# Optimization experiments

Hardware: AMD Instinct MI355X
Metric: run time of the kernel (lower is better)

## Reference

```python
import jax, jax.numpy as jnp
import numpy as np

B, C, T = 64, 8, 2048
K, DIL = 64, 1
NF = 32                      # n_frequencies (<= K//2+1 = 33)
MLP, HID = 32, 64
FFT_DIM = C * NF * 2         # 512
W = T - DIL * (K - 1)        # 1985 windows (== max_windows)


def setup_inputs() -> dict:
    key = jax.random.key(0)
    ks = jax.random.split(key, 12)
    s = 0.05
    return {
        "x": jax.random.normal(ks[0], (B, C, T), jnp.float32),
        "proj_w": jax.random.normal(ks[1], (MLP, FFT_DIM), jnp.float32) * s,
        "proj_b": jax.random.normal(ks[2], (MLP,), jnp.float32) * s,
        "w0": jax.random.normal(ks[3], (HID, MLP), jnp.float32) * s,      # Linear(32->64)
        "b0": jax.random.normal(ks[4], (HID,), jnp.float32) * s,
        "a0": jnp.ones((HID,), jnp.float32),                              # Snake a (a_init=1)
        "w1": jax.random.normal(ks[5], (MLP, HID), jnp.float32) * s,      # Linear(64->32)
        "b1": jax.random.normal(ks[6], (MLP,), jnp.float32) * s,
        "a1": jnp.ones((MLP,), jnp.float32),
        "wo": jax.random.normal(ks[7], (1, MLP), jnp.float32) * s,        # output Linear(32->1)
        "bo": jax.random.normal(ks[8], (1,), jnp.float32) * s,
        "agg": jax.random.normal(ks[9], (W,), jnp.float32) * s,           # agg_weights
    }


def _snake(x, a):
    aa = jnp.abs(a) + 1e-8
    return x + jnp.sin(aa * x) ** 2 / aa


def reference(x, proj_w, proj_b, w0, b0, a0, w1, b1, a1, wo, bo, agg):
    eff = DIL * (K - 1)
    # window t uses sorted indices t-(K-1)*DIL, ..., t  (step DIL)
    idx = eff + jnp.arange(W)[:, None] - (K - 1 - jnp.arange(K))[None, :] * DIL  # [W,K]
    win = x[:, :, idx]                                   # [B,C,W,K]
    fft = jnp.fft.rfft(win, axis=-1)[..., :NF]           # [B,C,W,NF] complex
    mag = jnp.log1p(jnp.abs(fft))
    ph = jnp.arctan2(fft.imag, fft.real) / np.pi
    feat = jnp.stack([mag, ph], axis=-1)                 # [B,C,W,NF,2]
    feat = jnp.transpose(feat, (0, 2, 1, 3, 4)).reshape(B, W, FFT_DIM)
    proj = jnp.tanh(feat @ proj_w.T + proj_b) * np.pi    # [B,W,MLP]
    h = _snake(proj @ w0.T + b0, a0)                     # [B,W,HID]
    h = _snake(h @ w1.T + b1, a1)                        # [B,W,MLP]
    out_t = (h @ wo.T + bo)[..., 0]                      # [B,W]
    wts = jax.nn.softmax(agg)                            # [W]
    return jnp.sum(out_t * wts, axis=1)                  # [B]
```

## Files before the change

kernel.cpp:

```cpp
#include <hip/hip_runtime.h>
#include <math.h>

#define B_ 64
#define C_ 8
#define T_ 2048
#define NF_ 32
#define MLP_ 32
#define HID_ 64
#define W_ 1985
#define CH_ 32
#define NCHUNK_ 63
#define PI_F 3.14159265358979323846f

typedef _Float16 f16x8 __attribute__((ext_vector_type(8)));
typedef _Float16 f16x2 __attribute__((ext_vector_type(2)));
typedef float    f32x4 __attribute__((ext_vector_type(4)));

#define WS_PARTIAL 64
#define WS_TWHI    4096
#define WS_TWLO    6144
#define WS_PWHI    8192
#define WS_PWLO    16384
#define WS_W0HI    24576
#define WS_W0LO    25600
#define WS_W1HI    26624
#define WS_W1LO    27648

__device__ __forceinline__ float fast_rcp(float x) { return __builtin_amdgcn_rcpf(x); }

__device__ __forceinline__ float fast_atan2pi(float y, float x)
{
    const float ax = fabsf(x), ay = fabsf(y);
    const float mx = fmaxf(ax, ay), mn = fminf(ax, ay);
    const float r  = mn * fast_rcp(fmaxf(mx, 1e-30f));
    const float t  = r * r;
    float a = -0.003730950f;
    a = fmaf(a, t,  0.016759940f);
    a = fmaf(a, t, -0.037059946f);
    a = fmaf(a, t,  0.061602941f);
    a = fmaf(a, t, -0.105877528f);
    a = fmaf(a, t,  0.318302656f);
    a *= r;
    a = (ay > ax) ? (0.5f - a) : a;
    a = (x < 0.0f) ? (1.0f - a) : a;
    return copysignf(a, y);
}

__device__ __forceinline__ float fast_tanh(float x)
{
    const float e = __expf(2.0f * x);
    return 1.0f - 2.0f * fast_rcp(e + 1.0f);
}

__device__ __forceinline__ float fast_snake(float h, float rcp_aa, float aa)
{
    const float s = __sinf(aa * h);
    return h + s * s * rcp_aa;
}

__device__ __forceinline__ float dot4(float4 a, float4 b, float acc)
{
    return fmaf(a.x, b.x, fmaf(a.y, b.y, fmaf(a.z, b.z, fmaf(a.w, b.w, acc))));
}

__device__ __forceinline__ unsigned packhl(float v)
{
    const _Float16 h = (_Float16)v;
    const _Float16 l = (_Float16)(v - (float)h);
    f16x2 p; p[0] = h; p[1] = l;
    return __builtin_bit_cast(unsigned, p);
}

__device__ __forceinline__ void unpack8(const unsigned* u, f16x8& ah, f16x8& al)
{
    union { unsigned w[4]; f16x8 v; } H, L;
    #pragma unroll
    for (int j = 0; j < 4; ++j) {
        H.w[j] = __builtin_amdgcn_perm(u[2*j+1], u[2*j], 0x05040100u);
        L.w[j] = __builtin_amdgcn_perm(u[2*j+1], u[2*j], 0x07060302u);
    }
    ah = H.v; al = L.v;
}

__device__ __forceinline__ void gload_lds16(const void* g, void* l)
{
    __builtin_amdgcn_global_load_lds(
        (const __attribute__((address_space(1))) void*)g,
        (__attribute__((address_space(3))) void*)l, 16, 0, 0);
}

__global__ __launch_bounds__(1024) void k_pre(
    const float* __restrict__ agg, const float* __restrict__ pw,
    const float* __restrict__ w0g, const float* __restrict__ w1g,
    float* __restrict__ ws)
{
    __shared__ float red[1024];
    const int t = threadIdx.x;

    _Float16* twHi = (_Float16*)(ws + WS_TWHI);
    _Float16* twLo = (_Float16*)(ws + WS_TWLO);
    #pragma unroll
    for (int e = 0; e < 4; ++e) {
        const int id = t * 4 + e;
        const int n = id >> 6, k = id & 63;
        const int f = n & 31;
        float s, c;
        sincosf(0.0981747704246810387f * (float)((k * f) & 63), &s, &c);
        const float v = (n < 32) ? c : -s;
        const _Float16 h = (_Float16)v;
        twHi[id] = h;
        twLo[id] = (_Float16)(v - (float)h);
    }

    _Float16* pwHi = (_Float16*)(ws + WS_PWHI);
    _Float16* pwLo = (_Float16*)(ws + WS_PWLO);
    #pragma unroll
    for (int e = 0; e < 16; ++e) {
        const int id = e * 1024 + t;
        const float v = pw[id];
        const _Float16 h = (_Float16)v;
        pwHi[id] = h;
        pwLo[id] = (_Float16)(v - (float)h);
    }

    _Float16* w0Hi = (_Float16*)(ws + WS_W0HI);
    _Float16* w0Lo = (_Float16*)(ws + WS_W0LO);
    _Float16* w1Hi = (_Float16*)(ws + WS_W1HI);
    _Float16* w1Lo = (_Float16*)(ws + WS_W1LO);
    #pragma unroll
    for (int e = 0; e < 2; ++e) {
        const int id = e * 1024 + t;
        const float v0 = w0g[id];
        const _Float16 h0 = (_Float16)v0;
        w0Hi[id] = h0;
        w0Lo[id] = (_Float16)(v0 - (float)h0);
        const float v1 = w1g[id];
        const _Float16 h1 = (_Float16)v1;
        w1Hi[id] = h1;
        w1Lo[id] = (_Float16)(v1 - (float)h1);
    }

    float m = -1e30f;
    for (int i = t; i < W_; i += 1024) m = fmaxf(m, agg[i]);
    red[t] = m;
    __syncthreads();
    for (int s = 512; s > 0; s >>= 1) {
        if (t < s) red[t] = fmaxf(red[t], red[t + s]);
        __syncthreads();
    }
    const float mx = red[0];
    __syncthreads();
    float sum = 0.f;
    for (int i = t; i < W_; i += 1024) sum += __expf(agg[i] - mx);
    red[t] = sum;
    __syncthreads();
    for (int s = 512; s > 0; s >>= 1) {
        if (t < s) red[t] += red[t + s];
        __syncthreads();
    }
    if (t == 0) { ws[0] = mx; ws[1] = red[0]; }
}

__global__ __launch_bounds__(1024, 8) void k_main(
    const float* __restrict__ x,  const float* __restrict__ pw,
    const float* __restrict__ pb, const float* __restrict__ w0g,
    const float* __restrict__ b0g,const float* __restrict__ a0g,
    const float* __restrict__ w1g,const float* __restrict__ b1g,
    const float* __restrict__ a1g,const float* __restrict__ wog,
    const float* __restrict__ bog,const float* __restrict__ agg,
    const float* __restrict__ wsp, float* __restrict__ partial)
{
    __shared__ __align__(16) _Float16 twHiL[4096];
    __shared__ __align__(16) _Float16 twLoL[4096];
    __shared__ __align__(16) _Float16 featP[16384];
    __shared__ __align__(16) _Float16 projP[2560];
    __shared__ __align__(16) _Float16 h0P[4608];
    __shared__ __align__(16) unsigned xtileP[C_][100];
    __shared__ float smalls[260];
    __shared__ float chunkAcc[CH_];

    _Float16* featHi = featP;
    _Float16* featLo = featP + 8192;
    _Float16* projHi = projP;
    _Float16* projLo = projP + 1280;
    _Float16* h0Hi   = h0P;
    _Float16* h0Lo   = h0P + 2304;
    float* pacc = (float*)featP;
    float* h1L  = (float*)featP;

    const int t     = threadIdx.x;
    const int chunk = blockIdx.x;
    const int b     = blockIdx.y;
    const int w0c   = chunk * CH_;
    const int wid   = t >> 6;
    const int lane  = t & 63;
    const int m16   = lane & 15;
    const int kl    = lane >> 4;
    const int cdft  = wid >> 1;

    {
        const int gl = (wid & 7) * 64 + lane;
        const int n  = gl >> 3, q = gl & 7;
        const int srcg = n * 8 + (q ^ (n & 7));
        const float* srcbase = wsp + ((wid < 8) ? WS_TWHI : WS_TWLO);
        _Float16* dst = ((wid < 8) ? twHiL : twLoL) + gl * 8;
        gload_lds16((const char*)srcbase + srcg * 16, dst);
    }

    if (t < C_ * 96) {
        const int c = t / 96;
        const int j = t - c * 96;
        int gi = w0c + j; if (gi > T_ - 1) gi = T_ - 1;
        xtileP[c][j] = packhl(x[((size_t)b * C_ + c) * T_ + gi]);
    }
    if (t < 257) {
        float smv;
        if      (t <  32) smv = pb[t];
        else if (t <  96) smv = b0g[t - 32];
        else if (t < 160) smv = a0g[t - 96];
        else if (t < 192) smv = b1g[t - 160];
        else if (t < 224) smv = a1g[t - 192];
        else if (t < 256) smv = wog[t - 224];
        else              smv = bog[0];
        smalls[t] = smv;
    }
    __syncthreads();

    f32x4 dacc0 = {0.f,0.f,0.f,0.f}, dacc1 = {0.f,0.f,0.f,0.f};
    f32x4 dacc2 = {0.f,0.f,0.f,0.f}, dacc3 = {0.f,0.f,0.f,0.f};
    const int wra = (wid & 1) * 16 + m16;
    {
        #pragma unroll
        for (int kstep = 0; kstep < 2; ++kstep) {
            const int kq = kstep * 4 + kl;
            unsigned ut[8];
            #pragma unroll
            for (int j = 0; j < 8; ++j) ut[j] = xtileP[cdft][wra + kq * 8 + j];
            f16x8 ah, al; unpack8(ut, ah, al);
            f32x4* dp[4] = { &dacc0, &dacc1, &dacc2, &dacc3 };
            #pragma unroll
            for (int nt = 0; nt < 4; ++nt) {
                const int nrow = nt * 16 + m16;
                const int gB = (nrow * 8 + (kq ^ (nrow & 7))) * 8;
                const f16x8 bh = *(const f16x8*)&twHiL[gB];
                const f16x8 bl = *(const f16x8*)&twLoL[gB];
                f32x4 a = *dp[nt];
                a = __builtin_amdgcn_mfma_f32_16x16x32_f16(ah, bh, a, 0, 0, 0);
                a = __builtin_amdgcn_mfma_f32_16x16x32_f16(al, bh, a, 0, 0, 0);
                a = __builtin_amdgcn_mfma_f32_16x16x32_f16(ah, bl, a, 0, 0, 0);
                *dp[nt] = a;
            }
        }
    }

    unsigned heldHi[2][4], heldLo[2][4];
    {
        const int wbase = (wid & 1) * 16 + kl * 4;
        const int ccl   = cdft & 3;
        const float reA[2][4] = {{dacc0[0],dacc0[1],dacc0[2],dacc0[3]},
                                 {dacc1[0],dacc1[1],dacc1[2],dacc1[3]}};
        const float imA[2][4] = {{dacc2[0],dacc2[1],dacc2[2],dacc2[3]},
                                 {dacc3[0],dacc3[1],dacc3[2],dacc3[3]}};
        #pragma unroll
        for (int fi = 0; fi < 2; ++fi) {
            const int f = fi * 16 + m16;
            const int g = ccl * 8 + (f >> 2);
            const int sub = 2 * (f & 3);
            #pragma unroll
            for (int r = 0; r < 4; ++r) {
                const int w  = wbase + r;
                const float re = reA[fi][r], im = imA[fi][r];
                const float mag = __logf(1.0f + __builtin_amdgcn_sqrtf(re*re + im*im));
                const float ph  = fast_atan2pi(im, re);
                const _Float16 mh = (_Float16)mag;
                const _Float16 qh = (_Float16)ph;
                f16x2 vh; vh[0] = mh; vh[1] = qh;
                f16x2 vl;
                vl[0] = (_Float16)(mag - (float)mh);
                vl[1] = (_Float16)(ph  - (float)qh);
                if (wid < 8) {
                    const int off = w * 256 + ((g ^ (w & 7)) * 8) + sub;
                    *(f16x2*)&featHi[off] = vh;
                    *(f16x2*)&featLo[off] = vl;
                } else {
                    heldHi[fi][r] = __builtin_bit_cast(unsigned, vh);
                    heldLo[fi][r] = __builtin_bit_cast(unsigned, vl);
                }
            }
        }
    }
    __syncthreads();

    const _Float16* pwHi = (const _Float16*)(wsp + WS_PWHI);
    const _Float16* pwLo = (const _Float16*)(wsp + WS_PWLO);
    {
        const int wt = (wid >> 1) & 1;
        const int ot = wid & 1;
        const int kq4 = wid >> 2;
        const int arow = wt * 16 + m16;
        const int brow = ot * 16 + m16;
        f32x4 acc = {0.f, 0.f, 0.f, 0.f};
        #pragma unroll
        for (int p = 0; p < 2; ++p) {
            #pragma unroll
            for (int kstep = 0; kstep < 2; ++kstep) {
                const int kp = kq4 * 64 + kstep * 32 + kl * 8;
                const f16x8 bh = *(const f16x8*)&pwHi[(size_t)brow * 512 + p * 256 + kp];
                const f16x8 bl = *(const f16x8*)&pwLo[(size_t)brow * 512 + p * 256 + kp];
                const int g0 = kp >> 3;
                const int offA = arow * 256 + ((g0 ^ (arow & 7)) * 8);
                const f16x8 ah = *(const f16x8*)&featHi[offA];
                const f16x8 al = *(const f16x8*)&featLo[offA];
                acc = __builtin_amdgcn_mfma_f32_16x16x32_f16(ah, bh, acc, 0, 0, 0);
                acc = __builtin_amdgcn_mfma_f32_16x16x32_f16(al, bh, acc, 0, 0, 0);
                acc = __builtin_amdgcn_mfma_f32_16x16x32_f16(ah, bl, acc, 0, 0, 0);
            }
            if (p == 0) {
                __syncthreads();
                if (wid >= 8) {
                    const int wbase = (wid & 1) * 16 + kl * 4;
                    const int ccl   = cdft & 3;
                    #pragma unroll
                    for (int fi = 0; fi < 2; ++fi) {
                        const int f = fi * 16 + m16;
                        const int g = ccl * 8 + (f >> 2);
                        const int sub = 2 * (f & 3);
                        #pragma unroll
                        for (int r = 0; r < 4; ++r) {
                            const int w  = wbase + r;
                            const int off = w * 256 + ((g ^ (w & 7)) * 8) + sub;
                            *(unsigned*)&featHi[off] = heldHi[fi][r];
                            *(unsigned*)&featLo[off] = heldLo[fi][r];
                        }
                    }
                }
                __syncthreads();
            }
        }
        __syncthreads();
        #pragma unroll
        for (int r = 0; r < 4; ++r) {
            const int w = wt * 16 + kl * 4 + r;
            const int o = ot * 16 + m16;
            pacc[kq4 * 1056 + w * 33 + o] = acc[r];
        }
    }
    __syncthreads();

    {
        const int o = t & 31;
        const int w = t >> 5;
        float s = smalls[o];
        #pragma unroll
        for (int q = 0; q < 4; ++q) s += pacc[q * 1056 + w * 33 + o];
        const float pr = fast_tanh(s) * PI_F;
        const _Float16 h = (_Float16)pr;
        projHi[w * 40 + o] = h;
        projLo[w * 40 + o] = (_Float16)(pr - (float)h);
    }
    __syncthreads();

    const _Float16* w0Hi = (const _Float16*)(wsp + WS_W0HI);
    const _Float16* w0Lo = (const _Float16*)(wsp + WS_W0LO);
    if (wid < 8) {
        const int wt = wid & 1;
        const int ot = wid >> 1;
        const int arow = wt * 16 + m16;
        const int brow = ot * 16 + m16;
        const f16x8 ah = *(const f16x8*)&projHi[arow * 40 + kl * 8];
        const f16x8 al = *(const f16x8*)&projLo[arow * 40 + kl * 8];
        const f16x8 bh = *(const f16x8*)&w0Hi[brow * 32 + kl * 8];
        const f16x8 bl = *(const f16x8*)&w0Lo[brow * 32 + kl * 8];
        f32x4 acc = {0.f, 0.f, 0.f, 0.f};
        acc = __builtin_amdgcn_mfma_f32_16x16x32_f16(ah, bh, acc, 0, 0, 0);
        acc = __builtin_amdgcn_mfma_f32_16x16x32_f16(al, bh, acc, 0, 0, 0);
        acc = __builtin_amdgcn_mfma_f32_16x16x32_f16(ah, bl, acc, 0, 0, 0);
        const int o  = ot * 16 + m16;
        const float b0v = smalls[32 + o];
        const float aa  = fabsf(smalls[96 + o]) + 1e-8f;
        const float ra  = fast_rcp(aa);
        #pragma unroll
        for (int r = 0; r < 4; ++r) {
            const int w = wt * 16 + kl * 4 + r;
            const float hv = fast_snake(acc[r] + b0v, ra, aa);
            const _Float16 h = (_Float16)hv;
            h0Hi[w * 72 + o] = h;
            h0Lo[w * 72 + o] = (_Float16)(hv - (float)h);
        }
    }
    __syncthreads();

    const _Float16* w1Hi = (const _Float16*)(wsp + WS_W1HI);
    const _Float16* w1Lo = (const _Float16*)(wsp + WS_W1LO);
    if (wid < 4) {
        const int wt = wid & 1;
        const int ot = wid >> 1;
        const int arow = wt * 16 + m16;
        const int brow = ot * 16 + m16;
        f32x4 acc = {0.f, 0.f, 0.f, 0.f};
        #pragma unroll
        for (int ks = 0; ks < 2; ++ks) {
            const f16x8 ah = *(const f16x8*)&h0Hi[arow * 72 + ks * 32 + kl * 8];
            const f16x8 al = *(const f16x8*)&h0Lo[arow * 72 + ks * 32 + kl * 8];
            const f16x8 bh = *(const f16x8*)&w1Hi[brow * 64 + ks * 32 + kl * 8];
            const f16x8 bl = *(const f16x8*)&w1Lo[brow * 64 + ks * 32 + kl * 8];
            acc = __builtin_amdgcn_mfma_f32_16x16x32_f16(ah, bh, acc, 0, 0, 0);
            acc = __builtin_amdgcn_mfma_f32_16x16x32_f16(al, bh, acc, 0, 0, 0);
            acc = __builtin_amdgcn_mfma_f32_16x16x32_f16(ah, bl, acc, 0, 0, 0);
        }
        const int o  = ot * 16 + m16;
        const float b1v = smalls[160 + o];
        const float aa  = fabsf(smalls[192 + o]) + 1e-8f;
        const float ra  = fast_rcp(aa);
        #pragma unroll
        for (int r = 0; r < 4; ++r) {
            const int w = wt * 16 + kl * 4 + r;
            h1L[w * 36 + o] = fast_snake(acc[r] + b1v, ra, aa);
        }
    }
    __syncthreads();

    if (t < CH_) {
        const int w = t;
        float acc = 0.f;
        #pragma unroll
        for (int q = 0; q < 8; ++q)
            acc = dot4(*(const float4*)&h1L[w * 36 + q * 4],
                       *(const float4*)&smalls[224 + q * 4], acc);
        const float val = acc + smalls[256];
        const int wg = w0c + w;
        const float sw = (wg < W_) ? __expf(agg[wg] - wsp[0]) / wsp[1] : 0.f;
        chunkAcc[w] = val * sw;
    }
    __syncthreads();

    if (t < 32) {
        float vs = chunkAcc[t];
        vs += __shfl_down(vs, 16);
        vs += __shfl_down(vs, 8);
        vs += __shfl_down(vs, 4);
        vs += __shfl_down(vs, 2);
        vs += __shfl_down(vs, 1);
        if (t == 0) partial[(size_t)chunk * B_ + b] = vs;
    }
}

__global__ void k_reduce(const float* __restrict__ partial, float* __restrict__ out)
{
    const int b = threadIdx.x;
    if (b < B_) {
        float s = 0.f;
        for (int c = 0; c < NCHUNK_; ++c) s += partial[(size_t)c * B_ + b];
        out[b] = s;
    }
}

extern "C" void kernel_launch(void* const* d_in, const int* in_sizes, int n_in,
                              void* d_out, int out_size, void* d_ws, size_t ws_size,
                              hipStream_t stream)
{
    const float* x   = (const float*)d_in[0];
    const float* pw  = (const float*)d_in[1];
    const float* pb  = (const float*)d_in[2];
    const float* w0  = (const float*)d_in[3];
    const float* b0  = (const float*)d_in[4];
    const float* a0  = (const float*)d_in[5];
    const float* w1  = (const float*)d_in[6];
    const float* b1  = (const float*)d_in[7];
    const float* a1  = (const float*)d_in[8];
    const float* wo  = (const float*)d_in[9];
    const float* bo  = (const float*)d_in[10];
    const float* agg = (const float*)d_in[11];
    float* ws  = (float*)d_ws;
    float* out = (float*)d_out;

    k_pre<<<1, 1024, 0, stream>>>(agg, pw, w0, w1, ws);
    dim3 grid(NCHUNK_, B_);
    k_main<<<grid, 1024, 0, stream>>>(x, pw, pb, w0, b0, a0, w1, b1, a1, wo, bo,
                                      agg, ws, ws + WS_PARTIAL);
    k_reduce<<<1, 64, 0, stream>>>(ws + WS_PARTIAL, out);
}
```

Before: 122.6 us.

## Halve block size, drop LDS twiddle staging, and alias buffers into feature tile

Changes the main kernel from 1024 to 512 threads per block. Each wave now processes two channels in sequence, alternating the DFT MFMA stage with a partial projection GEMM per channel pair. Twiddles are read straight from global/L2 instead of being copied into LDS with global_load_lds, and the proj/h0 buffers are aliased into the feature buffer to cut LDS per block. The aim is more resident blocks per CU and less LDS traffic. The cost is more barriers, serialised per-wave work, and unswizzled global twiddle reads.

```diff
diff --git a/kernel.cpp b/kernel.cpp
--- a/kernel.cpp
+++ b/kernel.cpp
@@ -82,13 +82,6 @@
     ah = H.v; al = L.v;
 }
 
-__device__ __forceinline__ void gload_lds16(const void* g, void* l)
-{
-    __builtin_amdgcn_global_load_lds(
-        (const __attribute__((address_space(1))) void*)g,
-        (__attribute__((address_space(3))) void*)l, 16, 0, 0);
-}
-
 __global__ __launch_bounds__(1024) void k_pre(
     const float* __restrict__ agg, const float* __restrict__ pw,
     const float* __restrict__ w0g, const float* __restrict__ w1g,
@@ -161,7 +154,7 @@
     if (t == 0) { ws[0] = mx; ws[1] = red[0]; }
 }
 
-__global__ __launch_bounds__(1024, 8) void k_main(
+__global__ __launch_bounds__(512, 8) void k_main(
     const float* __restrict__ x,  const float* __restrict__ pw,
     const float* __restrict__ pb, const float* __restrict__ w0g,
     const float* __restrict__ b0g,const float* __restrict__ a0g,
@@ -170,23 +163,19 @@
     const float* __restrict__ bog,const float* __restrict__ agg,
     const float* __restrict__ wsp, float* __restrict__ partial)
 {
-    __shared__ __align__(16) _Float16 twHiL[4096];
-    __shared__ __align__(16) _Float16 twLoL[4096];
     __shared__ __align__(16) _Float16 featP[16384];
-    __shared__ __align__(16) _Float16 projP[2560];
-    __shared__ __align__(16) _Float16 h0P[4608];
     __shared__ __align__(16) unsigned xtileP[C_][100];
     __shared__ float smalls[260];
     __shared__ float chunkAcc[CH_];
 
     _Float16* featHi = featP;
     _Float16* featLo = featP + 8192;
-    _Float16* projHi = projP;
-    _Float16* projLo = projP + 1280;
-    _Float16* h0Hi   = h0P;
-    _Float16* h0Lo   = h0P + 2304;
-    float* pacc = (float*)featP;
-    float* h1L  = (float*)featP;
+    float*    pacc   = (float*)featP;
+    _Float16* projHi = featP + 4224;
+    _Float16* projLo = featP + 4224 + 1280;
+    _Float16* h0Hi   = featP + 6784;
+    _Float16* h0Lo   = featP + 6784 + 2304;
+    float*    h1L    = (float*)featP;
 
     const int t     = threadIdx.x;
     const int chunk = blockIdx.x;
@@ -196,20 +185,10 @@
     const int lane  = t & 63;
     const int m16   = lane & 15;
     const int kl    = lane >> 4;
-    const int cdft  = wid >> 1;
-
-    {
-        const int gl = (wid & 7) * 64 + lane;
-        const int n  = gl >> 3, q = gl & 7;
-        const int srcg = n * 8 + (q ^ (n & 7));
-        const float* srcbase = wsp + ((wid < 8) ? WS_TWHI : WS_TWLO);
-        _Float16* dst = ((wid < 8) ? twHiL : twLoL) + gl * 8;
-        gload_lds16((const char*)srcbase + srcg * 16, dst);
-    }
-
-    if (t < C_ * 96) {
-        const int c = t / 96;
-        const int j = t - c * 96;
+
+    for (int i = t; i < C_ * 100; i += 512) {
+        const int c = i / 100;
+        const int j = i - c * 100;
         int gi = w0c + j; if (gi > T_ - 1) gi = T_ - 1;
         xtileP[c][j] = packhl(x[((size_t)b * C_ + c) * T_ + gi]);
     }
@@ -226,133 +205,125 @@
     }
     __syncthreads();
 
-    f32x4 dacc0 = {0.f,0.f,0.f,0.f}, dacc1 = {0.f,0.f,0.f,0.f};
-    f32x4 dacc2 = {0.f,0.f,0.f,0.f}, dacc3 = {0.f,0.f,0.f,0.f};
-    const int wra = (wid & 1) * 16 + m16;
-    {
+    const _Float16* twHig = (const _Float16*)(wsp + WS_TWHI);
+    const _Float16* twLog = (const _Float16*)(wsp + WS_TWLO);
+    const _Float16* pwHi  = (const _Float16*)(wsp + WS_PWHI);
+    const _Float16* pwLo  = (const _Float16*)(wsp + WS_PWLO);
+
+    const int cdl = wid >> 1;
+    const int wh  = wid & 1;
+    const int wra = wh * 16 + m16;
+    const int gwt = (wid >> 1) & 1;
+    const int got = wid & 1;
+    const int gkq = wid >> 2;
+    const int garow = gwt * 16 + m16;
+    const int gbrow = got * 16 + m16;
+    f32x4 acc = {0.f, 0.f, 0.f, 0.f};
+
+    #pragma unroll
+    for (int p = 0; p < 2; ++p) {
+        const int c = p * 4 + cdl;
+        f32x4 d0 = {0.f,0.f,0.f,0.f}, d1 = {0.f,0.f,0.f,0.f};
+        f32x4 d2 = {0.f,0.f,0.f,0.f}, d3 = {0.f,0.f,0.f,0.f};
         #pragma unroll
         for (int kstep = 0; kstep < 2; ++kstep) {
             const int kq = kstep * 4 + kl;
             unsigned ut[8];
             #pragma unroll
-            for (int j = 0; j < 8; ++j) ut[j] = xtileP[cdft][wra + kq * 8 + j];
+            for (int j = 0; j < 8; ++j) ut[j] = xtileP[c][wra + kq * 8 + j];
             f16x8 ah, al; unpack8(ut, ah, al);
-            f32x4* dp[4] = { &dacc0, &dacc1, &dacc2, &dacc3 };
+            {
+                const f16x8 bh = *(const f16x8*)&twHig[(m16     ) * 64 + kq * 8];
+                const f16x8 bl = *(const f16x8*)&twLog[(m16     ) * 64 + kq * 8];
+                d0 = __builtin_amdgcn_mfma_f32_16x16x32_f16(ah, bh, d0, 0, 0, 0);
+                d0 = __builtin_amdgcn_mfma_f32_16x16x32_f16(al, bh, d0, 0, 0, 0);
+                d0 = __builtin_amdgcn_mfma_f32_16x16x32_f16(ah, bl, d0, 0, 0, 0);
+            }
+            {
+                const f16x8 bh = *(const f16x8*)&twHig[(16 + m16) * 64 + kq * 8];
+                const f16x8 bl = *(const f16x8*)&twLog[(16 + m16) * 64 + kq * 8];
+                d1 = __builtin_amdgcn_mfma_f32_16x16x32_f16(ah, bh, d1, 0, 0, 0);
+                d1 = __builtin_amdgcn_mfma_f32_16x16x32_f16(al, bh, d1, 0, 0, 0);
+                d1 = __builtin_amdgcn_mfma_f32_16x16x32_f16(ah, bl, d1, 0, 0, 0);
+            }
+            {
+                const f16x8 bh = *(const f16x8*)&twHig[(32 + m16) * 64 + kq * 8];
+                const f16x8 bl = *(const f16x8*)&twLog[(32 + m16) * 64 + kq * 8];
+                d2 = __builtin_amdgcn_mfma_f32_16x16x32_f16(ah, bh, d2, 0, 0, 0);
+                d2 = __builtin_amdgcn_mfma_f32_16x16x32_f16(al, bh, d2, 0, 0, 0);
+                d2 = __builtin_amdgcn_mfma_f32_16x16x32_f16(ah, bl, d2, 0, 0, 0);
+            }
+            {
+                const f16x8 bh = *(const f16x8*)&twHig[(48 + m16) * 64 + kq * 8];
+                const f16x8 bl = *(const f16x8*)&twLog[(48 + m16) * 64 + kq * 8];
+                d3 = __builtin_amdgcn_mfma_f32_16x16x32_f16(ah, bh, d3, 0, 0, 0);
+                d3 = __builtin_amdgcn_mfma_f32_16x16x32_f16(al, bh, d3, 0, 0, 0);
+                d3 = __builtin_amdgcn_mfma_f32_16x16x32_f16(ah, bl, d3, 0, 0, 0);
+            }
+        }
+
+        {
+            const int cl = c & 3;
+            const int wbase = wh * 16 + kl * 4;
+            const float reA[2][4] = {{d0[0],d0[1],d0[2],d0[3]},
+                                     {d1[0],d1[1],d1[2],d1[3]}};
+            const float imA[2][4] = {{d2[0],d2[1],d2[2],d2[3]},
+                                     {d3[0],d3[1],d3[2],d3[3]}};
             #pragma unroll
-            for (int nt = 0; nt < 4; ++nt) {
-                const int nrow = nt * 16 + m16;
-                const int gB = (nrow * 8 + (kq ^ (nrow & 7))) * 8;
-                const f16x8 bh = *(const f16x8*)&twHiL[gB];
-                const f16x8 bl = *(const f16x8*)&twLoL[gB];
-                f32x4 a = *dp[nt];
-                a = __builtin_amdgcn_mfma_f32_16x16x32_f16(ah, bh, a, 0, 0, 0);
-                a = __builtin_amdgcn_mfma_f32_16x16x32_f16(al, bh, a, 0, 0, 0);
-                a = __builtin_amdgcn_mfma_f32_16x16x32_f16(ah, bl, a, 0, 0, 0);
-                *dp[nt] = a;
-            }
-        }
-    }
-
-    unsigned heldHi[2][4], heldLo[2][4];
-    {
-        const int wbase = (wid & 1) * 16 + kl * 4;
-        const int ccl   = cdft & 3;
-        const float reA[2][4] = {{dacc0[0],dacc0[1],dacc0[2],dacc0[3]},
-                                 {dacc1[0],dacc1[1],dacc1[2],dacc1[3]}};
-        const float imA[2][4] = {{dacc2[0],dacc2[1],dacc2[2],dacc2[3]},
-                                 {dacc3[0],dacc3[1],dacc3[2],dacc3[3]}};
-        #pragma unroll
-        for (int fi = 0; fi < 2; ++fi) {
-            const int f = fi * 16 + m16;
-            const int g = ccl * 8 + (f >> 2);
-            const int sub = 2 * (f & 3);
-            #pragma unroll
-            for (int r = 0; r < 4; ++r) {
-                const int w  = wbase + r;
-                const float re = reA[fi][r], im = imA[fi][r];
-                const float mag = __logf(1.0f + __builtin_amdgcn_sqrtf(re*re + im*im));
-                const float ph  = fast_atan2pi(im, re);
-                const _Float16 mh = (_Float16)mag;
-                const _Float16 qh = (_Float16)ph;
-                f16x2 vh; vh[0] = mh; vh[1] = qh;
-                f16x2 vl;
-                vl[0] = (_Float16)(mag - (float)mh);
-                vl[1] = (_Float16)(ph  - (float)qh);
-                if (wid < 8) {
+            for (int fi = 0; fi < 2; ++fi) {
+                const int f = fi * 16 + m16;
+                const int g = cl * 8 + (f >> 2);
+                const int sub = 2 * (f & 3);
+                #pragma unroll
+                for (int r = 0; r < 4; ++r) {
+                    const int w = wbase + r;
+                    const float re = reA[fi][r], im = imA[fi][r];
+                    const float mag = __logf(1.0f + __builtin_amdgcn_sqrtf(re*re + im*im));
+                    const float ph  = fast_atan2pi(im, re);
+                    const _Float16 mh = (_Float16)mag;
+                    const _Float16 qh = (_Float16)ph;
+                    f16x2 vh; vh[0] = mh; vh[1] = qh;
+                    f16x2 vl;
+                    vl[0] = (_Float16)(mag - (float)mh);
+                    vl[1] = (_Float16)(ph  - (float)qh);
                     const int off = w * 256 + ((g ^ (w & 7)) * 8) + sub;
                     *(f16x2*)&featHi[off] = vh;
                     *(f16x2*)&featLo[off] = vl;
-                } else {
-                    heldHi[fi][r] = __builtin_bit_cast(unsigned, vh);
-                    heldLo[fi][r] = __builtin_bit_cast(unsigned, vl);
                 }
             }
         }
-    }
-    __syncthreads();
-
-    const _Float16* pwHi = (const _Float16*)(wsp + WS_PWHI);
-    const _Float16* pwLo = (const _Float16*)(wsp + WS_PWLO);
-    {
-        const int wt = (wid >> 1) & 1;
-        const int ot = wid & 1;
-        const int kq4 = wid >> 2;
-        const int arow = wt * 16 + m16;
-        const int brow = ot * 16 + m16;
-        f32x4 acc = {0.f, 0.f, 0.f, 0.f};
-        #pragma unroll
-        for (int p = 0; p < 2; ++p) {
-            #pragma unroll
-            for (int kstep = 0; kstep < 2; ++kstep) {
-                const int kp = kq4 * 64 + kstep * 32 + kl * 8;
-                const f16x8 bh = *(const f16x8*)&pwHi[(size_t)brow * 512 + p * 256 + kp];
-                const f16x8 bl = *(const f16x8*)&pwLo[(size_t)brow * 512 + p * 256 + kp];
-                const int g0 = kp >> 3;
-                const int offA = arow * 256 + ((g0 ^ (arow & 7)) * 8);
-                const f16x8 ah = *(const f16x8*)&featHi[offA];
-                const f16x8 al = *(const f16x8*)&featLo[offA];
-                acc = __builtin_amdgcn_mfma_f32_16x16x32_f16(ah, bh, acc, 0, 0, 0);
-                acc = __builtin_amdgcn_mfma_f32_16x16x32_f16(al, bh, acc, 0, 0, 0);
-                acc = __builtin_amdgcn_mfma_f32_16x16x32_f16(ah, bl, acc, 0, 0, 0);
-            }
-            if (p == 0) {
-                __syncthreads();
-                if (wid >= 8) {
-                    const int wbase = (wid & 1) * 16 + kl * 4;
-                    const int ccl   = cdft & 3;
-                    #pragma unroll
-                    for (int fi = 0; fi < 2; ++fi) {
-                        const int f = fi * 16 + m16;
-                        const int g = ccl * 8 + (f >> 2);
-                        const int sub = 2 * (f & 3);
-                        #pragma unroll
-                        for (int r = 0; r < 4; ++r) {
-                            const int w  = wbase + r;
-                            const int off = w * 256 + ((g ^ (w & 7)) * 8) + sub;
-                            *(unsigned*)&featHi[off] = heldHi[fi][r];
-                            *(unsigned*)&featLo[off] = heldLo[fi][r];
-                        }
-                    }
-                }
-                __syncthreads();
-            }
-        }
         __syncthreads();
-        #pragma unroll
-        for (int r = 0; r < 4; ++r) {
-            const int w = wt * 16 + kl * 4 + r;
-            const int o = ot * 16 + m16;
-            pacc[kq4 * 1056 + w * 33 + o] = acc[r];
-        }
-    }
-    __syncthreads();
-
-    {
-        const int o = t & 31;
-        const int w = t >> 5;
-        float s = smalls[o];
-        #pragma unroll
-        for (int q = 0; q < 4; ++q) s += pacc[q * 1056 + w * 33 + o];
+
+        #pragma unroll
+        for (int kstep = 0; kstep < 4; ++kstep) {
+            const int kloc = gkq * 128 + kstep * 32 + kl * 8;
+            const f16x8 bh = *(const f16x8*)&pwHi[(size_t)gbrow * 512 + p * 256 + kloc];
+            const f16x8 bl = *(const f16x8*)&pwLo[(size_t)gbrow * 512 + p * 256 + kloc];
+            const int g0 = kloc >> 3;
+            const int offA = garow * 256 + ((g0 ^ (garow & 7)) * 8);
+            const f16x8 ah = *(const f16x8*)&featHi[offA];
+            const f16x8 al = *(const f16x8*)&featLo[offA];
+            acc = __builtin_amdgcn_mfma_f32_16x16x32_f16(ah, bh, acc, 0, 0, 0);
+            acc = __builtin_amdgcn_mfma_f32_16x16x32_f16(al, bh, acc, 0, 0, 0);
+            acc = __builtin_amdgcn_mfma_f32_16x16x32_f16(ah, bl, acc, 0, 0, 0);
+        }
+        __syncthreads();
+    }
+
+    #pragma unroll
+    for (int r = 0; r < 4; ++r) {
+        const int w = gwt * 16 + kl * 4 + r;
+        const int o = got * 16 + m16;
+        pacc[gkq * 1056 + w * 33 + o] = acc[r];
+    }
+    __syncthreads();
+
+    #pragma unroll
+    for (int q2 = 0; q2 < 2; ++q2) {
+        const int idx = t + q2 * 512;
+        const int o = idx & 31;
+        const int w = idx >> 5;
+        const float s = smalls[o] + pacc[w * 33 + o] + pacc[1056 + w * 33 + o];
         const float pr = fast_tanh(s) * PI_F;
         const _Float16 h = (_Float16)pr;
         projHi[w * 40 + o] = h;
@@ -362,7 +333,7 @@
 
     const _Float16* w0Hi = (const _Float16*)(wsp + WS_W0HI);
     const _Float16* w0Lo = (const _Float16*)(wsp + WS_W0LO);
-    if (wid < 8) {
+    {
         const int wt = wid & 1;
         const int ot = wid >> 1;
         const int arow = wt * 16 + m16;
@@ -371,10 +342,10 @@
         const f16x8 al = *(const f16x8*)&projLo[arow * 40 + kl * 8];
         const f16x8 bh = *(const f16x8*)&w0Hi[brow * 32 + kl * 8];
         const f16x8 bl = *(const f16x8*)&w0Lo[brow * 32 + kl * 8];
-        f32x4 acc = {0.f, 0.f, 0.f, 0.f};
-        acc = __builtin_amdgcn_mfma_f32_16x16x32_f16(ah, bh, acc, 0, 0, 0);
-        acc = __builtin_amdgcn_mfma_f32_16x16x32_f16(al, bh, acc, 0, 0, 0);
-        acc = __builtin_amdgcn_mfma_f32_16x16x32_f16(ah, bl, acc, 0, 0, 0);
+        f32x4 hacc = {0.f, 0.f, 0.f, 0.f};
+        hacc = __builtin_amdgcn_mfma_f32_16x16x32_f16(ah, bh, hacc, 0, 0, 0);
+        hacc = __builtin_amdgcn_mfma_f32_16x16x32_f16(al, bh, hacc, 0, 0, 0);
+        hacc = __builtin_amdgcn_mfma_f32_16x16x32_f16(ah, bl, hacc, 0, 0, 0);
         const int o  = ot * 16 + m16;
         const float b0v = smalls[32 + o];
         const float aa  = fabsf(smalls[96 + o]) + 1e-8f;
@@ -382,7 +353,7 @@
         #pragma unroll
         for (int r = 0; r < 4; ++r) {
             const int w = wt * 16 + kl * 4 + r;
-            const float hv = fast_snake(acc[r] + b0v, ra, aa);
+            const float hv = fast_snake(hacc[r] + b0v, ra, aa);
             const _Float16 h = (_Float16)hv;
             h0Hi[w * 72 + o] = h;
             h0Lo[w * 72 + o] = (_Float16)(hv - (float)h);
@@ -397,16 +368,16 @@
         const int ot = wid >> 1;
         const int arow = wt * 16 + m16;
         const int brow = ot * 16 + m16;
-        f32x4 acc = {0.f, 0.f, 0.f, 0.f};
+        f32x4 hacc = {0.f, 0.f, 0.f, 0.f};
         #pragma unroll
         for (int ks = 0; ks < 2; ++ks) {
             const f16x8 ah = *(const f16x8*)&h0Hi[arow * 72 + ks * 32 + kl * 8];
             const f16x8 al = *(const f16x8*)&h0Lo[arow * 72 + ks * 32 + kl * 8];
             const f16x8 bh = *(const f16x8*)&w1Hi[brow * 64 + ks * 32 + kl * 8];
             const f16x8 bl = *(const f16x8*)&w1Lo[brow * 64 + ks * 32 + kl * 8];
-            acc = __builtin_amdgcn_mfma_f32_16x16x32_f16(ah, bh, acc, 0, 0, 0);
-            acc = __builtin_amdgcn_mfma_f32_16x16x32_f16(al, bh, acc, 0, 0, 0);
-            acc = __builtin_amdgcn_mfma_f32_16x16x32_f16(ah, bl, acc, 0, 0, 0);
+            hacc = __builtin_amdgcn_mfma_f32_16x16x32_f16(ah, bh, hacc, 0, 0, 0);
+            hacc = __builtin_amdgcn_mfma_f32_16x16x32_f16(al, bh, hacc, 0, 0, 0);
+            hacc = __builtin_amdgcn_mfma_f32_16x16x32_f16(ah, bl, hacc, 0, 0, 0);
         }
         const int o  = ot * 16 + m16;
         const float b1v = smalls[160 + o];
@@ -415,19 +386,19 @@
         #pragma unroll
         for (int r = 0; r < 4; ++r) {
             const int w = wt * 16 + kl * 4 + r;
-            h1L[w * 36 + o] = fast_snake(acc[r] + b1v, ra, aa);
+            h1L[w * 36 + o] = fast_snake(hacc[r] + b1v, ra, aa);
         }
     }
     __syncthreads();
 
     if (t < CH_) {
         const int w = t;
-        float acc = 0.f;
+        float acc2 = 0.f;
         #pragma unroll
         for (int q = 0; q < 8; ++q)
-            acc = dot4(*(const float4*)&h1L[w * 36 + q * 4],
-                       *(const float4*)&smalls[224 + q * 4], acc);
-        const float val = acc + smalls[256];
+            acc2 = dot4(*(const float4*)&h1L[w * 36 + q * 4],
+                        *(const float4*)&smalls[224 + q * 4], acc2);
+        const float val = acc2 + smalls[256];
         const int wg = w0c + w;
         const float sw = (wg < W_) ? __expf(agg[wg] - wsp[0]) / wsp[1] : 0.f;
         chunkAcc[w] = val * sw;
@@ -476,7 +447,7 @@
 
     k_pre<<<1, 1024, 0, stream>>>(agg, pw, w0, w1, ws);
     dim3 grid(NCHUNK_, B_);
-    k_main<<<grid, 1024, 0, stream>>>(x, pw, pb, w0, b0, a0, w1, b1, a1, wo, bo,
-                                      agg, ws, ws + WS_PARTIAL);
+    k_main<<<grid, 512, 0, stream>>>(x, pw, pb, w0, b0, a0, w1, b1, a1, wo, bo,
+                                     agg, ws, ws + WS_PARTIAL);
     k_reduce<<<1, 64, 0, stream>>>(ws + WS_PARTIAL, out);
 }
```

Result: slower. 209.8 us (+71.2%).

## Stage first half of projection weights in LDS and parallelize weight prep

Applied to the files above, without the earlier changes.

The projection-weight hi/lo split in the prep kernel is spread across 8 blocks instead of one, while only block 0 keeps doing the twiddle and other setup. In the main kernel, LDS is reorganised into an arena so that, once the DFT stage finishes, the first half of the hi/lo projection weights is loaded asynchronously into swizzled LDS, reusing the twiddle and x-tile space. The p=0 projection pass reads its B operands from LDS instead of global memory. This adds a block-wide barrier and changes LDS aliasing of the proj/h0 buffers, which could affect occupancy and correctness.

```diff
diff --git a/kernel.cpp b/kernel.cpp
--- a/kernel.cpp
+++ b/kernel.cpp
@@ -95,7 +95,21 @@
     float* __restrict__ ws)
 {
     __shared__ float red[1024];
-    const int t = threadIdx.x;
+    const int t   = threadIdx.x;
+    const int blk = blockIdx.x;
+
+    _Float16* pwHi = (_Float16*)(ws + WS_PWHI);
+    _Float16* pwLo = (_Float16*)(ws + WS_PWLO);
+    #pragma unroll
+    for (int e = 0; e < 2; ++e) {
+        const int id = blk * 2048 + e * 1024 + t;
+        const float v = pw[id];
+        const _Float16 h = (_Float16)v;
+        pwHi[id] = h;
+        pwLo[id] = (_Float16)(v - (float)h);
+    }
+
+    if (blk != 0) return;
 
     _Float16* twHi = (_Float16*)(ws + WS_TWHI);
     _Float16* twLo = (_Float16*)(ws + WS_TWLO);
@@ -110,17 +124,6 @@
         const _Float16 h = (_Float16)v;
         twHi[id] = h;
         twLo[id] = (_Float16)(v - (float)h);
-    }
-
-    _Float16* pwHi = (_Float16*)(ws + WS_PWHI);
-    _Float16* pwLo = (_Float16*)(ws + WS_PWLO);
-    #pragma unroll
-    for (int e = 0; e < 16; ++e) {
-        const int id = e * 1024 + t;
-        const float v = pw[id];
-        const _Float16 h = (_Float16)v;
-        pwHi[id] = h;
-        pwLo[id] = (_Float16)(v - (float)h);
     }
 
     _Float16* w0Hi = (_Float16*)(ws + WS_W0HI);
@@ -170,23 +173,24 @@
     const float* __restrict__ bog,const float* __restrict__ agg,
     const float* __restrict__ wsp, float* __restrict__ partial)
 {
-    __shared__ __align__(16) _Float16 twHiL[4096];
-    __shared__ __align__(16) _Float16 twLoL[4096];
     __shared__ __align__(16) _Float16 featP[16384];
-    __shared__ __align__(16) _Float16 projP[2560];
-    __shared__ __align__(16) _Float16 h0P[4608];
-    __shared__ __align__(16) unsigned xtileP[C_][100];
+    __shared__ __align__(16) _Float16 arena2[16384];
     __shared__ float smalls[260];
     __shared__ float chunkAcc[CH_];
 
     _Float16* featHi = featP;
     _Float16* featLo = featP + 8192;
-    _Float16* projHi = projP;
-    _Float16* projLo = projP + 1280;
-    _Float16* h0Hi   = h0P;
-    _Float16* h0Lo   = h0P + 2304;
-    float* pacc = (float*)featP;
-    float* h1L  = (float*)featP;
+    _Float16* twHiL  = arena2;
+    _Float16* twLoL  = arena2 + 4096;
+    unsigned* xtileP = (unsigned*)(arena2 + 8192);
+    _Float16* pw0Hi  = arena2;
+    _Float16* pw0Lo  = arena2 + 8192;
+    float*    pacc   = (float*)featP;
+    _Float16* projHi = featP + 8448;
+    _Float16* projLo = featP + 8448 + 1280;
+    _Float16* h0Hi   = featP + 11008;
+    _Float16* h0Lo   = featP + 11008 + 2304;
+    float*    h1L    = (float*)featP;
 
     const int t     = threadIdx.x;
     const int chunk = blockIdx.x;
@@ -211,7 +215,7 @@
         const int c = t / 96;
         const int j = t - c * 96;
         int gi = w0c + j; if (gi > T_ - 1) gi = T_ - 1;
-        xtileP[c][j] = packhl(x[((size_t)b * C_ + c) * T_ + gi]);
+        xtileP[c * 100 + j] = packhl(x[((size_t)b * C_ + c) * T_ + gi]);
     }
     if (t < 257) {
         float smv;
@@ -235,7 +239,7 @@
             const int kq = kstep * 4 + kl;
             unsigned ut[8];
             #pragma unroll
-            for (int j = 0; j < 8; ++j) ut[j] = xtileP[cdft][wra + kq * 8 + j];
+            for (int j = 0; j < 8; ++j) ut[j] = xtileP[cdft * 100 + wra + kq * 8 + j];
             f16x8 ah, al; unpack8(ut, ah, al);
             f32x4* dp[4] = { &dacc0, &dacc1, &dacc2, &dacc3 };
             #pragma unroll
@@ -250,6 +254,23 @@
                 a = __builtin_amdgcn_mfma_f32_16x16x32_f16(ah, bl, a, 0, 0, 0);
                 *dp[nt] = a;
             }
+        }
+    }
+    __syncthreads();
+
+    {
+        const char* pwbytes = (const char*)wsp;
+        #pragma unroll
+        for (int r = 0; r < 2; ++r) {
+            const int gw = (r * 16 + wid) * 64;
+            const int g  = gw + lane;
+            const int plane = g >> 10;
+            const int gp = g & 1023;
+            const int o  = gp >> 5;
+            const int q  = gp & 31;
+            const size_t srcoff = (size_t)(plane ? WS_PWLO : WS_PWHI) * 4
+                                + (size_t)o * 1024 + (size_t)((q ^ (o & 7)) * 16);
+            gload_lds16(pwbytes + srcoff, (char*)arena2 + (size_t)g * 16);
         }
     }
 
@@ -305,8 +326,15 @@
             #pragma unroll
             for (int kstep = 0; kstep < 2; ++kstep) {
                 const int kp = kq4 * 64 + kstep * 32 + kl * 8;
-                const f16x8 bh = *(const f16x8*)&pwHi[(size_t)brow * 512 + p * 256 + kp];
-                const f16x8 bl = *(const f16x8*)&pwLo[(size_t)brow * 512 + p * 256 + kp];
+                f16x8 bh, bl;
+                if (p == 0) {
+                    const int offB = brow * 256 + (((kp >> 3) ^ (brow & 7)) * 8);
+                    bh = *(const f16x8*)&pw0Hi[offB];
+                    bl = *(const f16x8*)&pw0Lo[offB];
+                } else {
+                    bh = *(const f16x8*)&pwHi[(size_t)brow * 512 + 256 + kp];
+                    bl = *(const f16x8*)&pwLo[(size_t)brow * 512 + 256 + kp];
+                }
                 const int g0 = kp >> 3;
                 const int offA = arow * 256 + ((g0 ^ (arow & 7)) * 8);
                 const f16x8 ah = *(const f16x8*)&featHi[offA];
@@ -474,7 +502,7 @@
     float* ws  = (float*)d_ws;
     float* out = (float*)d_out;
 
-    k_pre<<<1, 1024, 0, stream>>>(agg, pw, w0, w1, ws);
+    k_pre<<<8, 1024, 0, stream>>>(agg, pw, w0, w1, ws);
     dim3 grid(NCHUNK_, B_);
     k_main<<<grid, 1024, 0, stream>>>(x, pw, pb, w0, b0, a0, w1, b1, a1, wo, bo,
                                       agg, ws, ws + WS_PARTIAL);
```

Result: faster. 112.7 us (-8.1%).
